# Optimization experiments

Measured on AMD Instinct MI355X. Metric: run time of the kernel, lower is better.

## Reference

```python
import jax, jax.numpy as jnp
import numpy as np

H = 256   # hidden_dim
S = 16    # d_state
B = 2
N = 8192
LN_EPS = 1e-5


def setup_inputs() -> dict:
    key = jax.random.key(0)
    ks = jax.random.split(key, 12)
    std = 1.0 / np.sqrt(H)
    inp = {
        'x': jax.random.normal(ks[0], (B, N, H), dtype=jnp.float32),
        'in_w': jax.random.normal(ks[1], (2 * H, H), dtype=jnp.float32) * std,
        'in_b': jax.random.normal(ks[2], (2 * H,), dtype=jnp.float32) * std,
        'xp_w': jax.random.normal(ks[3], (2 * S + 1, H), dtype=jnp.float32) * std,
        'xp_b': jax.random.normal(ks[4], (2 * S + 1,), dtype=jnp.float32) * std,
        'dt_w': jax.random.normal(ks[5], (H, 1), dtype=jnp.float32),
        'dt_b': jax.random.normal(ks[6], (H,), dtype=jnp.float32),
        'A_log': jnp.log(jnp.broadcast_to(jnp.arange(1, S + 1, dtype=jnp.float32), (H, S))),
        'D': jnp.ones((H,), dtype=jnp.float32),
        'out_w': jax.random.normal(ks[7], (H, H), dtype=jnp.float32) * std,
        'out_b': jax.random.normal(ks[8], (H,), dtype=jnp.float32) * std,
        'ln_g': jnp.ones((H,), dtype=jnp.float32),
        'ln_b': jnp.zeros((H,), dtype=jnp.float32),
    }
    return inp


def reference(x, in_w, in_b, xp_w, xp_b, dt_w, dt_b, A_log, D, out_w, out_b, ln_g, ln_b):
    # x: (B, N, H). Dropout is identity in eval mode.
    residual = x
    xz = jnp.einsum('bnh,kh->bnk', x, in_w) + in_b            # (B,N,2H)
    x_inner, z = xz[..., :H], xz[..., H:]
    x_dbl = jnp.einsum('bnh,kh->bnk', x_inner, xp_w) + xp_b   # (B,N,2S+1)
    dt_raw = x_dbl[..., :1]
    B_raw = x_dbl[..., 1:S + 1]                               # (B,N,S)
    C_raw = x_dbl[..., S + 1:]                                # (B,N,S)
    dt = jax.nn.softplus(dt_raw * dt_w[:, 0] + dt_b)          # (B,N,H)
    # NOTE: the original computes dA = exp(dt * A) but never uses it; A_log
    # does not affect the output, so we skip materializing dA.
    dB = dt[..., None] * B_raw[:, :, None, :]                 # (B,N,H,S)
    h = jnp.cumsum(x_inner[..., None] * dB, axis=1)           # (B,N,H,S)
    y = jnp.einsum('bnhs,bns->bnh', h, C_raw) + D * x_inner   # (B,N,H)
    y = y * jax.nn.silu(z)
    out = jnp.einsum('bnh,kh->bnk', y, out_w) + out_b
    r = out + residual
    mu = jnp.mean(r, axis=-1, keepdims=True)
    var = jnp.mean((r - mu) ** 2, axis=-1, keepdims=True)
    return ln_g * (r - mu) * jax.lax.rsqrt(var + LN_EPS) + ln_b
```

## Files before the change

kernel.cpp:

```cpp
#include <hip/hip_runtime.h>
#include <hip/hip_bf16.h>


#define HD 256
#define SD 16
#define NSEQ 8192
#define NBATCH 2
#define BN (NBATCH * NSEQ)
#define CHUNK 32
#define NCHUNK (NSEQ / CHUNK)
#define NGRP 16
#define GSZ (NCHUNK / NGRP)
#define LN_EPS 1e-5f

#define NIW (2 * HD * HD)
#define NXP (48 * HD)
#define NOW (HD * HD)

typedef __hip_bfloat16 bf16;
typedef __attribute__((ext_vector_type(8))) short bf16x8;
typedef __attribute__((ext_vector_type(4))) short short4v;
typedef __attribute__((ext_vector_type(4))) float f32x4;

__device__ __forceinline__ float b2f(bf16 v) { return __bfloat162float(v); }
__device__ __forceinline__ short f2bs(float f) {
  union { bf16 b; short s; } u;
  u.b = __float2bfloat16(f);
  return u.s;
}
__device__ __forceinline__ bf16x8 cvt_frag(const float* p) {
  bf16x8 r;
#pragma unroll
  for (int j = 0; j < 8; ++j) r[j] = f2bs(p[j]);
  return r;
}
__device__ __forceinline__ float softplus_f(float a) {
  return (a > 20.f) ? a : __logf(1.f + __expf(a));
}

__global__ __launch_bounds__(256) void k0_weights(
    const float* __restrict__ in_w, const float* __restrict__ xp_w,
    const float* __restrict__ out_w, bf16* __restrict__ wbin,
    bf16* __restrict__ wbxp, bf16* __restrict__ wbout)
{
  const int base = (blockIdx.x * 256 + threadIdx.x) * 4;
  if (base < NIW) {
    f32x4 v = *(const f32x4*)(in_w + base);
    *(short4v*)((short*)wbin + base) =
        short4v{f2bs(v[0]), f2bs(v[1]), f2bs(v[2]), f2bs(v[3])};
  } else if (base < NIW + NXP) {
    const int off = base - NIW;
    short4v s;
    if (off < 33 * HD) {
      f32x4 v = *(const f32x4*)(xp_w + off);
      s = short4v{f2bs(v[0]), f2bs(v[1]), f2bs(v[2]), f2bs(v[3])};
    } else {
      s = short4v{0, 0, 0, 0};
    }
    *(short4v*)((short*)wbxp + off) = s;
  } else if (base < NIW + NXP + NOW) {
    const int off = base - NIW - NXP;
    f32x4 v = *(const f32x4*)(out_w + off);
    *(short4v*)((short*)wbout + off) =
        short4v{f2bs(v[0]), f2bs(v[1]), f2bs(v[2]), f2bs(v[3])};
  }
}

__global__ __launch_bounds__(256) void k1f_in_xp_sum(
    const float* __restrict__ x, const bf16* __restrict__ wbin,
    const float* __restrict__ in_b, const bf16* __restrict__ wbxp,
    const float* __restrict__ xp_b, const float* __restrict__ dt_w,
    const float* __restrict__ dt_b, bf16* __restrict__ xib,
    bf16* __restrict__ zb, float* __restrict__ dbc, float* __restrict__ Mc)
{
  __shared__ float tile[32][260];
  __shared__ float sdbc[32][33];
  const int tid = threadIdx.x;
  const int wave = tid >> 6, lane = tid & 63, q = lane >> 4, l16 = lane & 15;
  const int R0 = blockIdx.x * CHUNK;

  f32x4 acc[2][8] = {};
  {
    const float* a0 = x + (size_t)(R0 + l16) * HD + q * 8;
    const float* a1 = a0 + 16 * HD;
    const bf16* bp = wbin + (size_t)(wave * 128 + l16) * HD + q * 8;
#pragma unroll
    for (int k = 0; k < HD; k += 32) {
      bf16x8 af0 = cvt_frag(a0 + k);
      bf16x8 af1 = cvt_frag(a1 + k);
#pragma unroll
      for (int t = 0; t < 8; ++t) {
        bf16x8 bfr = *(const bf16x8*)(bp + (size_t)t * 16 * HD + k);
        acc[0][t] = __builtin_amdgcn_mfma_f32_16x16x32_bf16(af0, bfr, acc[0][t], 0, 0, 0);
        acc[1][t] = __builtin_amdgcn_mfma_f32_16x16x32_bf16(af1, bfr, acc[1][t], 0, 0, 0);
      }
    }
  }
  if (wave < 2) {
#pragma unroll
    for (int t = 0; t < 8; ++t) {
      const int col = wave * 128 + t * 16 + l16;
      const float bias = in_b[col];
#pragma unroll
      for (int rt = 0; rt < 2; ++rt)
#pragma unroll
        for (int r = 0; r < 4; ++r)
          tile[rt * 16 + q * 4 + r][col] = acc[rt][t][r] + bias;
    }
  }
  __syncthreads();

  {
    const int row = tid >> 3;
    const int cb = (tid & 7) * 8;
#pragma unroll
    for (int j = 0; j < 4; ++j) {
      bf16x8 v = cvt_frag(&tile[row][cb + j * 64]);
      *(bf16x8*)(xib + (size_t)(R0 + row) * HD + cb + j * 64) = v;
    }
  }
  f32x4 pacc[3] = {};
  if (wave < 2) {
    const bf16* pb = wbxp + (size_t)l16 * HD + q * 8;
#pragma unroll
    for (int k = 0; k < HD; k += 32) {
      bf16x8 af = cvt_frag(&tile[wave * 16 + l16][k + q * 8]);
#pragma unroll
      for (int t = 0; t < 3; ++t) {
        bf16x8 bfr = *(const bf16x8*)(pb + (size_t)t * 16 * HD + k);
        pacc[t] = __builtin_amdgcn_mfma_f32_16x16x32_bf16(af, bfr, pacc[t], 0, 0, 0);
      }
    }
#pragma unroll
    for (int t = 0; t < 3; ++t) {
      const int col = t * 16 + l16;
      if (col < 33) {
        const float bias = xp_b[col];
#pragma unroll
        for (int r = 0; r < 4; ++r)
          sdbc[wave * 16 + q * 4 + r][col] = pacc[t][r] + bias;
      }
    }
  }
  __syncthreads();

  {
    const float* sflat = &sdbc[0][0];
    for (int idx = tid; idx < CHUNK * 33; idx += 256)
      dbc[(size_t)R0 * 33 + idx] = sflat[idx];
  }
  {
    const int h = tid;
    const float dtw = dt_w[h], dtb = dt_b[h];
    float st[SD] = {};
#pragma unroll
    for (int n = 0; n < CHUNK; ++n) {
      const float xv = tile[n][h];
      const float dt = softplus_f(sdbc[n][0] * dtw + dtb);
      const float u = xv * dt;
#pragma unroll
      for (int s = 0; s < SD; ++s) st[s] += u * sdbc[n][1 + s];
    }
    const int b = R0 >> 13, c = (R0 & (NSEQ - 1)) >> 5;
    float* mp = Mc + ((size_t)(b * NCHUNK + c)) * 4096 + h;
#pragma unroll
    for (int s = 0; s < SD; ++s) mp[s * HD] = st[s];
  }
  __syncthreads();

  if (wave >= 2) {
#pragma unroll
    for (int t = 0; t < 8; ++t) {
      const int gcol = wave * 128 + t * 16 + l16;
      const float bias = in_b[gcol];
      const int col = gcol - 256;
#pragma unroll
      for (int rt = 0; rt < 2; ++rt)
#pragma unroll
        for (int r = 0; r < 4; ++r)
          tile[rt * 16 + q * 4 + r][col] = acc[rt][t][r] + bias;
    }
  }
  __syncthreads();
  {
    const int row = tid >> 3;
    const int cb = (tid & 7) * 8;
#pragma unroll
    for (int j = 0; j < 4; ++j) {
      bf16x8 v = cvt_frag(&tile[row][cb + j * 64]);
      *(bf16x8*)(zb + (size_t)(R0 + row) * HD + cb + j * 64) = v;
    }
  }
}

__global__ __launch_bounds__(256) void k4a_prefix_local(
    float* __restrict__ Mc, float* __restrict__ Gs)
{
  const int tid = blockIdx.x * 256 + threadIdx.x;
  const int b = tid >> 16;
  const int g = (tid >> 12) & (NGRP - 1);
  const int hs = tid & 4095;
  float run = 0.f;
#pragma unroll
  for (int i = 0; i < GSZ; ++i) {
    const size_t idx = ((size_t)(b * NCHUNK + g * GSZ + i)) * 4096 + hs;
    const float v = Mc[idx];
    Mc[idx] = run;
    run += v;
  }
  Gs[((size_t)(b * NGRP + g)) * 4096 + hs] = run;
}

__global__ __launch_bounds__(256) void k4b_prefix_groups(float* __restrict__ Gs)
{
  const int tid = blockIdx.x * 256 + threadIdx.x;
  const int b = tid >> 12;
  const int hs = tid & 4095;
  float run = 0.f;
#pragma unroll
  for (int g = 0; g < NGRP; ++g) {
    const size_t idx = ((size_t)(b * NGRP + g)) * 4096 + hs;
    const float v = Gs[idx];
    Gs[idx] = run;
    run += v;
  }
}

__global__ __launch_bounds__(256) void k56_scan_out_ln(
    const bf16* __restrict__ xib, const bf16* __restrict__ zb,
    const float* __restrict__ dbc, const float* __restrict__ dt_w,
    const float* __restrict__ dt_b, const float* __restrict__ Dv,
    const float* __restrict__ Mc, const float* __restrict__ Gs,
    const bf16* __restrict__ wbout, const float* __restrict__ out_b,
    const float* __restrict__ x, const float* __restrict__ ln_g,
    const float* __restrict__ ln_b, float* __restrict__ out)
{
  __shared__ float sdbc[CHUNK][33];
  __shared__ float ytile[32][264];
  const int tid = threadIdx.x;
  const int R0 = blockIdx.x * CHUNK;
  const int b = R0 >> 13;
  const int cchunk = (R0 & (NSEQ - 1)) >> 5;

  for (int idx = tid; idx < CHUNK * 33; idx += 256) {
    const int n = idx / 33, j = idx - n * 33;
    sdbc[n][j] = dbc[(size_t)(R0 + n) * 33 + j];
  }
  __syncthreads();

  {
    const int h = tid;
    const float dtw = dt_w[h];
    const float dtb = dt_b[h];
    const float dv = Dv[h];
    float st[SD];
    const float* mp = Mc + ((size_t)(b * NCHUNK + cchunk)) * 4096 + h;
    const float* gp = Gs + ((size_t)(b * NGRP + cchunk / GSZ)) * 4096 + h;
#pragma unroll
    for (int s = 0; s < SD; ++s) st[s] = mp[s * HD] + gp[s * HD];
    for (int n = 0; n < CHUNK; ++n) {
      const size_t row = (size_t)(R0 + n) * HD + h;
      const float xv = b2f(xib[row]);
      const float zv = b2f(zb[row]);
      const float dt = softplus_f(sdbc[n][0] * dtw + dtb);
      const float u = xv * dt;
      float y = dv * xv;
#pragma unroll
      for (int s = 0; s < SD; ++s) {
        st[s] += u * sdbc[n][1 + s];
        y += st[s] * sdbc[n][17 + s];
      }
      const float sig = 1.f / (1.f + __expf(-zv));
      ytile[n][h] = y * zv * sig;
    }
  }
  __syncthreads();

  const int wave = tid >> 6;
  const int lane = tid & 63;
  const int q = lane >> 4;
  const int l16 = lane & 15;
  const int mrow = (wave & 1) * 16;
  const int colBase = (wave >> 1) * 128;

  f32x4 acc[8] = {};
  const bf16* bptr = wbout + (size_t)(colBase + l16) * HD + q * 8;
#pragma unroll
  for (int k = 0; k < HD; k += 32) {
    bf16x8 af = cvt_frag(&ytile[mrow + l16][k + q * 8]);
#pragma unroll
    for (int t = 0; t < 8; ++t) {
      bf16x8 bfr = *(const bf16x8*)(bptr + (size_t)t * 16 * HD + k);
      acc[t] = __builtin_amdgcn_mfma_f32_16x16x32_bf16(af, bfr, acc[t], 0, 0, 0);
    }
  }
  __syncthreads();

#pragma unroll
  for (int t = 0; t < 8; ++t) {
    const int col = colBase + t * 16 + l16;
    const float bias = out_b[col];
#pragma unroll
    for (int r = 0; r < 4; ++r) {
      const int row = mrow + q * 4 + r;
      ytile[row][col] = acc[t][r] + bias + x[(size_t)(R0 + row) * HD + col];
    }
  }
  __syncthreads();

#pragma unroll
  for (int rr = 0; rr < 8; ++rr) {
    const int row = wave * 8 + rr;
    float p = 0.f;
#pragma unroll
    for (int j = 0; j < 4; ++j) p += ytile[row][lane + 64 * j];
#pragma unroll
    for (int off = 32; off > 0; off >>= 1) p += __shfl_xor(p, off);
    const float mu = p * (1.f / 256.f);
    float v2 = 0.f;
#pragma unroll
    for (int j = 0; j < 4; ++j) {
      const float d = ytile[row][lane + 64 * j] - mu;
      v2 += d * d;
    }
#pragma unroll
    for (int off = 32; off > 0; off >>= 1) v2 += __shfl_xor(v2, off);
    const float rstd = rsqrtf(v2 * (1.f / 256.f) + LN_EPS);
    const size_t base = (size_t)(R0 + row) * HD;
#pragma unroll
    for (int j = 0; j < 4; ++j) {
      const int cc = lane + 64 * j;
      out[base + cc] = ln_g[cc] * (ytile[row][cc] - mu) * rstd + ln_b[cc];
    }
  }
}

extern "C" void kernel_launch(void* const* d_in, const int* in_sizes, int n_in,
                              void* d_out, int out_size, void* d_ws, size_t ws_size,
                              hipStream_t stream)
{
  const float* x     = (const float*)d_in[0];
  const float* in_w  = (const float*)d_in[1];
  const float* in_b  = (const float*)d_in[2];
  const float* xp_w  = (const float*)d_in[3];
  const float* xp_b  = (const float*)d_in[4];
  const float* dt_w  = (const float*)d_in[5];
  const float* dt_b  = (const float*)d_in[6];
  const float* Dv    = (const float*)d_in[8];
  const float* out_w = (const float*)d_in[9];
  const float* out_b = (const float*)d_in[10];
  const float* ln_g  = (const float*)d_in[11];
  const float* ln_b  = (const float*)d_in[12];

  char* ws = (char*)d_ws;
  bf16*  xib   = (bf16*)(ws);
  bf16*  zb    = (bf16*)(ws +  8388608);
  float* dbc   = (float*)(ws + 16777216);
  float* Mc    = (float*)(ws + 18939904);
  float* Gs    = (float*)(ws + 27328512);
  bf16*  wbin  = (bf16*)(ws + 27852800);
  bf16*  wbxp  = (bf16*)(ws + 28114944);
  bf16*  wbout = (bf16*)(ws + 28139520);
  float* out   = (float*)d_out;

  hipLaunchKernelGGL(k0_weights, dim3((NIW + NXP + NOW) / 1024), dim3(256),
                     0, stream, in_w, xp_w, out_w, wbin, wbxp, wbout);
  hipLaunchKernelGGL(k1f_in_xp_sum, dim3(BN / CHUNK), dim3(256), 0, stream,
                     x, wbin, in_b, wbxp, xp_b, dt_w, dt_b,
                     xib, zb, dbc, Mc);
  hipLaunchKernelGGL(k4a_prefix_local, dim3(NBATCH * NGRP * 4096 / 256),
                     dim3(256), 0, stream, Mc, Gs);
  hipLaunchKernelGGL(k4b_prefix_groups, dim3(NBATCH * 4096 / 256), dim3(256),
                     0, stream, Gs);
  hipLaunchKernelGGL(k56_scan_out_ln, dim3(BN / CHUNK), dim3(256), 0, stream,
                     xib, zb, dbc, dt_w, dt_b, Dv, Mc, Gs,
                     wbout, out_b, x, ln_g, ln_b, out);
}
```

Before: 167.5 us.

## Double block size to 512 threads, splitting state dimension across thread halves

Both the fused input-projection kernel and the scan/out-projection/LayerNorm kernel move from 256 to 512 threads per block. The 16 state channels are split between two thread halves, with partial y sums combined in shared memory. In the first kernel, x is staged in LDS and each wave computes a 16x128 tile, with x and z written through separate tiles. The goal is more parallelism and fewer serial state updates per thread, at the cost of more LDS per block, extra syncs and a reduction pass.

```diff
diff --git a/kernel.cpp b/kernel.cpp
--- a/kernel.cpp
+++ b/kernel.cpp
@@ -66,65 +66,78 @@
   }
 }
 
-__global__ __launch_bounds__(256) void k1f_in_xp_sum(
+__global__ __launch_bounds__(512) void k1f_in_xp_sum(
     const float* __restrict__ x, const bf16* __restrict__ wbin,
     const float* __restrict__ in_b, const bf16* __restrict__ wbxp,
     const float* __restrict__ xp_b, const float* __restrict__ dt_w,
     const float* __restrict__ dt_b, bf16* __restrict__ xib,
     bf16* __restrict__ zb, float* __restrict__ dbc, float* __restrict__ Mc)
 {
-  __shared__ float tile[32][260];
+  __shared__ float xt[32][260];
+  __shared__ float zt[32][260];
   __shared__ float sdbc[32][33];
   const int tid = threadIdx.x;
   const int wave = tid >> 6, lane = tid & 63, q = lane >> 4, l16 = lane & 15;
   const int R0 = blockIdx.x * CHUNK;
 
-  f32x4 acc[2][8] = {};
-  {
-    const float* a0 = x + (size_t)(R0 + l16) * HD + q * 8;
-    const float* a1 = a0 + 16 * HD;
-    const bf16* bp = wbin + (size_t)(wave * 128 + l16) * HD + q * 8;
+  {
+    const int row = tid >> 4;
+    const int c0 = (tid & 15) * 16;
+    const float* src = x + (size_t)(R0 + row) * HD + c0;
+#pragma unroll
+    for (int j = 0; j < 4; ++j)
+      *(f32x4*)&xt[row][c0 + j * 4] = *(const f32x4*)(src + j * 4);
+  }
+  __syncthreads();
+
+  const int mrow = (wave & 1) * 16;
+  const int colBase = (wave >> 1) * 128;
+  f32x4 acc[8] = {};
+  {
+    const bf16* bp = wbin + (size_t)(colBase + l16) * HD + q * 8;
 #pragma unroll
     for (int k = 0; k < HD; k += 32) {
-      bf16x8 af0 = cvt_frag(a0 + k);
-      bf16x8 af1 = cvt_frag(a1 + k);
+      bf16x8 af = cvt_frag(&xt[mrow + l16][k + q * 8]);
 #pragma unroll
       for (int t = 0; t < 8; ++t) {
         bf16x8 bfr = *(const bf16x8*)(bp + (size_t)t * 16 * HD + k);
-        acc[0][t] = __builtin_amdgcn_mfma_f32_16x16x32_bf16(af0, bfr, acc[0][t], 0, 0, 0);
-        acc[1][t] = __builtin_amdgcn_mfma_f32_16x16x32_bf16(af1, bfr, acc[1][t], 0, 0, 0);
-      }
-    }
-  }
+        acc[t] = __builtin_amdgcn_mfma_f32_16x16x32_bf16(af, bfr, acc[t], 0, 0, 0);
+      }
+    }
+  }
+  __syncthreads();
+
+  {
+    float (*dst)[260] = (wave < 4) ? xt : zt;
+    const int cb = (wave < 4) ? colBase : (colBase - 256);
+#pragma unroll
+    for (int t = 0; t < 8; ++t) {
+      const int gcol = colBase + t * 16 + l16;
+      const float bias = in_b[gcol];
+#pragma unroll
+      for (int r = 0; r < 4; ++r)
+        dst[mrow + q * 4 + r][cb + t * 16 + l16] = acc[t][r] + bias;
+    }
+  }
+  __syncthreads();
+
+  {
+    const int row = tid >> 4;
+    const int c0 = (tid & 15) * 16;
+    bf16* xd = xib + (size_t)(R0 + row) * HD + c0;
+    bf16* zd = zb + (size_t)(R0 + row) * HD + c0;
+    *(bf16x8*)xd = cvt_frag(&xt[row][c0]);
+    *(bf16x8*)(xd + 8) = cvt_frag(&xt[row][c0 + 8]);
+    *(bf16x8*)zd = cvt_frag(&zt[row][c0]);
+    *(bf16x8*)(zd + 8) = cvt_frag(&zt[row][c0 + 8]);
+  }
+
   if (wave < 2) {
-#pragma unroll
-    for (int t = 0; t < 8; ++t) {
-      const int col = wave * 128 + t * 16 + l16;
-      const float bias = in_b[col];
-#pragma unroll
-      for (int rt = 0; rt < 2; ++rt)
-#pragma unroll
-        for (int r = 0; r < 4; ++r)
-          tile[rt * 16 + q * 4 + r][col] = acc[rt][t][r] + bias;
-    }
-  }
-  __syncthreads();
-
-  {
-    const int row = tid >> 3;
-    const int cb = (tid & 7) * 8;
-#pragma unroll
-    for (int j = 0; j < 4; ++j) {
-      bf16x8 v = cvt_frag(&tile[row][cb + j * 64]);
-      *(bf16x8*)(xib + (size_t)(R0 + row) * HD + cb + j * 64) = v;
-    }
-  }
-  f32x4 pacc[3] = {};
-  if (wave < 2) {
+    f32x4 pacc[3] = {};
     const bf16* pb = wbxp + (size_t)l16 * HD + q * 8;
 #pragma unroll
     for (int k = 0; k < HD; k += 32) {
-      bf16x8 af = cvt_frag(&tile[wave * 16 + l16][k + q * 8]);
+      bf16x8 af = cvt_frag(&xt[wave * 16 + l16][k + q * 8]);
 #pragma unroll
       for (int t = 0; t < 3; ++t) {
         bf16x8 bfr = *(const bf16x8*)(pb + (size_t)t * 16 * HD + k);
@@ -146,50 +159,26 @@
 
   {
     const float* sflat = &sdbc[0][0];
-    for (int idx = tid; idx < CHUNK * 33; idx += 256)
+    for (int idx = tid; idx < CHUNK * 33; idx += 512)
       dbc[(size_t)R0 * 33 + idx] = sflat[idx];
   }
   {
-    const int h = tid;
+    const int h = tid & 255;
+    const int sh = tid >> 8;
     const float dtw = dt_w[h], dtb = dt_b[h];
-    float st[SD] = {};
+    float st[8] = {};
 #pragma unroll
     for (int n = 0; n < CHUNK; ++n) {
-      const float xv = tile[n][h];
+      const float xv = xt[n][h];
       const float dt = softplus_f(sdbc[n][0] * dtw + dtb);
       const float u = xv * dt;
 #pragma unroll
-      for (int s = 0; s < SD; ++s) st[s] += u * sdbc[n][1 + s];
+      for (int s = 0; s < 8; ++s) st[s] += u * sdbc[n][1 + sh * 8 + s];
     }
     const int b = R0 >> 13, c = (R0 & (NSEQ - 1)) >> 5;
-    float* mp = Mc + ((size_t)(b * NCHUNK + c)) * 4096 + h;
-#pragma unroll
-    for (int s = 0; s < SD; ++s) mp[s * HD] = st[s];
-  }
-  __syncthreads();
-
-  if (wave >= 2) {
-#pragma unroll
-    for (int t = 0; t < 8; ++t) {
-      const int gcol = wave * 128 + t * 16 + l16;
-      const float bias = in_b[gcol];
-      const int col = gcol - 256;
-#pragma unroll
-      for (int rt = 0; rt < 2; ++rt)
-#pragma unroll
-        for (int r = 0; r < 4; ++r)
-          tile[rt * 16 + q * 4 + r][col] = acc[rt][t][r] + bias;
-    }
-  }
-  __syncthreads();
-  {
-    const int row = tid >> 3;
-    const int cb = (tid & 7) * 8;
-#pragma unroll
-    for (int j = 0; j < 4; ++j) {
-      bf16x8 v = cvt_frag(&tile[row][cb + j * 64]);
-      *(bf16x8*)(zb + (size_t)(R0 + row) * HD + cb + j * 64) = v;
-    }
+    float* mp = Mc + ((size_t)(b * NCHUNK + c)) * 4096 + (sh * 8) * HD + h;
+#pragma unroll
+    for (int s = 0; s < 8; ++s) mp[s * HD] = st[s];
   }
 }
 
@@ -226,7 +215,7 @@
   }
 }
 
-__global__ __launch_bounds__(256) void k56_scan_out_ln(
+__global__ __launch_bounds__(512) void k56_scan_out_ln(
     const bf16* __restrict__ xib, const bf16* __restrict__ zb,
     const float* __restrict__ dbc, const float* __restrict__ dt_w,
     const float* __restrict__ dt_b, const float* __restrict__ Dv,
@@ -236,91 +225,101 @@
     const float* __restrict__ ln_b, float* __restrict__ out)
 {
   __shared__ float sdbc[CHUNK][33];
-  __shared__ float ytile[32][264];
+  __shared__ float yt[32][260];
+  __shared__ float pt[32][260];
   const int tid = threadIdx.x;
+  const int wave = tid >> 6, lane = tid & 63, q = lane >> 4, l16 = lane & 15;
   const int R0 = blockIdx.x * CHUNK;
   const int b = R0 >> 13;
   const int cchunk = (R0 & (NSEQ - 1)) >> 5;
 
-  for (int idx = tid; idx < CHUNK * 33; idx += 256) {
+  for (int idx = tid; idx < CHUNK * 33; idx += 512) {
     const int n = idx / 33, j = idx - n * 33;
     sdbc[n][j] = dbc[(size_t)(R0 + n) * 33 + j];
   }
   __syncthreads();
 
   {
-    const int h = tid;
-    const float dtw = dt_w[h];
-    const float dtb = dt_b[h];
+    const int h = tid & 255;
+    const int sh = tid >> 8;
+    const float dtw = dt_w[h], dtb = dt_b[h];
     const float dv = Dv[h];
-    float st[SD];
-    const float* mp = Mc + ((size_t)(b * NCHUNK + cchunk)) * 4096 + h;
-    const float* gp = Gs + ((size_t)(b * NGRP + cchunk / GSZ)) * 4096 + h;
-#pragma unroll
-    for (int s = 0; s < SD; ++s) st[s] = mp[s * HD] + gp[s * HD];
+    float st[8];
+    const float* mp = Mc + ((size_t)(b * NCHUNK + cchunk)) * 4096 + sh * 8 * HD + h;
+    const float* gp = Gs + ((size_t)(b * NGRP + cchunk / GSZ)) * 4096 + sh * 8 * HD + h;
+#pragma unroll
+    for (int s = 0; s < 8; ++s) st[s] = mp[s * HD] + gp[s * HD];
+    float (*dst)[260] = (sh == 0) ? yt : pt;
     for (int n = 0; n < CHUNK; ++n) {
-      const size_t row = (size_t)(R0 + n) * HD + h;
-      const float xv = b2f(xib[row]);
-      const float zv = b2f(zb[row]);
+      const float xv = b2f(xib[(size_t)(R0 + n) * HD + h]);
       const float dt = softplus_f(sdbc[n][0] * dtw + dtb);
       const float u = xv * dt;
-      float y = dv * xv;
-#pragma unroll
-      for (int s = 0; s < SD; ++s) {
-        st[s] += u * sdbc[n][1 + s];
-        y += st[s] * sdbc[n][17 + s];
-      }
+      float y = (sh == 0) ? dv * xv : 0.f;
+#pragma unroll
+      for (int s = 0; s < 8; ++s) {
+        st[s] += u * sdbc[n][1 + sh * 8 + s];
+        y += st[s] * sdbc[n][17 + sh * 8 + s];
+      }
+      dst[n][h] = y;
+    }
+  }
+  __syncthreads();
+
+  {
+    const int h = tid & 255;
+    const int r2 = tid >> 8;
+#pragma unroll
+    for (int j = 0; j < 16; ++j) {
+      const int row = r2 * 16 + j;
+      const float zv = b2f(zb[(size_t)(R0 + row) * HD + h]);
       const float sig = 1.f / (1.f + __expf(-zv));
-      ytile[n][h] = y * zv * sig;
-    }
-  }
-  __syncthreads();
-
-  const int wave = tid >> 6;
-  const int lane = tid & 63;
-  const int q = lane >> 4;
-  const int l16 = lane & 15;
+      yt[row][h] = (yt[row][h] + pt[row][h]) * zv * sig;
+    }
+  }
+  __syncthreads();
+
   const int mrow = (wave & 1) * 16;
-  const int colBase = (wave >> 1) * 128;
-
-  f32x4 acc[8] = {};
-  const bf16* bptr = wbout + (size_t)(colBase + l16) * HD + q * 8;
-#pragma unroll
-  for (int k = 0; k < HD; k += 32) {
-    bf16x8 af = cvt_frag(&ytile[mrow + l16][k + q * 8]);
-#pragma unroll
-    for (int t = 0; t < 8; ++t) {
-      bf16x8 bfr = *(const bf16x8*)(bptr + (size_t)t * 16 * HD + k);
-      acc[t] = __builtin_amdgcn_mfma_f32_16x16x32_bf16(af, bfr, acc[t], 0, 0, 0);
-    }
-  }
-  __syncthreads();
-
-#pragma unroll
-  for (int t = 0; t < 8; ++t) {
+  const int colBase = (wave >> 1) * 64;
+  f32x4 acc[4] = {};
+  {
+    const bf16* bp = wbout + (size_t)(colBase + l16) * HD + q * 8;
+#pragma unroll
+    for (int k = 0; k < HD; k += 32) {
+      bf16x8 af = cvt_frag(&yt[mrow + l16][k + q * 8]);
+#pragma unroll
+      for (int t = 0; t < 4; ++t) {
+        bf16x8 bfr = *(const bf16x8*)(bp + (size_t)t * 16 * HD + k);
+        acc[t] = __builtin_amdgcn_mfma_f32_16x16x32_bf16(af, bfr, acc[t], 0, 0, 0);
+      }
+    }
+  }
+  __syncthreads();
+
+#pragma unroll
+  for (int t = 0; t < 4; ++t) {
     const int col = colBase + t * 16 + l16;
     const float bias = out_b[col];
 #pragma unroll
     for (int r = 0; r < 4; ++r) {
       const int row = mrow + q * 4 + r;
-      ytile[row][col] = acc[t][r] + bias + x[(size_t)(R0 + row) * HD + col];
-    }
-  }
-  __syncthreads();
-
-#pragma unroll
-  for (int rr = 0; rr < 8; ++rr) {
-    const int row = wave * 8 + rr;
+      pt[row][col] = acc[t][r] + bias + x[(size_t)(R0 + row) * HD + col];
+    }
+  }
+  __syncthreads();
+
+#pragma unroll
+  for (int rr = 0; rr < 4; ++rr) {
+    const int row = wave * 4 + rr;
     float p = 0.f;
 #pragma unroll
-    for (int j = 0; j < 4; ++j) p += ytile[row][lane + 64 * j];
+    for (int j = 0; j < 4; ++j) p += pt[row][lane + 64 * j];
 #pragma unroll
     for (int off = 32; off > 0; off >>= 1) p += __shfl_xor(p, off);
     const float mu = p * (1.f / 256.f);
     float v2 = 0.f;
 #pragma unroll
     for (int j = 0; j < 4; ++j) {
-      const float d = ytile[row][lane + 64 * j] - mu;
+      const float d = pt[row][lane + 64 * j] - mu;
       v2 += d * d;
     }
 #pragma unroll
@@ -330,7 +329,7 @@
 #pragma unroll
     for (int j = 0; j < 4; ++j) {
       const int cc = lane + 64 * j;
-      out[base + cc] = ln_g[cc] * (ytile[row][cc] - mu) * rstd + ln_b[cc];
+      out[base + cc] = ln_g[cc] * (pt[row][cc] - mu) * rstd + ln_b[cc];
     }
   }
 }
@@ -365,14 +364,14 @@
 
   hipLaunchKernelGGL(k0_weights, dim3((NIW + NXP + NOW) / 1024), dim3(256),
                      0, stream, in_w, xp_w, out_w, wbin, wbxp, wbout);
-  hipLaunchKernelGGL(k1f_in_xp_sum, dim3(BN / CHUNK), dim3(256), 0, stream,
+  hipLaunchKernelGGL(k1f_in_xp_sum, dim3(BN / CHUNK), dim3(512), 0, stream,
                      x, wbin, in_b, wbxp, xp_b, dt_w, dt_b,
                      xib, zb, dbc, Mc);
   hipLaunchKernelGGL(k4a_prefix_local, dim3(NBATCH * NGRP * 4096 / 256),
                      dim3(256), 0, stream, Mc, Gs);
   hipLaunchKernelGGL(k4b_prefix_groups, dim3(NBATCH * 4096 / 256), dim3(256),
                      0, stream, Gs);
-  hipLaunchKernelGGL(k56_scan_out_ln, dim3(BN / CHUNK), dim3(256), 0, stream,
+  hipLaunchKernelGGL(k56_scan_out_ln, dim3(BN / CHUNK), dim3(512), 0, stream,
                      xib, zb, dbc, dt_w, dt_b, Dv, Mc, Gs,
                      wbout, out_b, x, ln_g, ln_b, out);
 }
```

After: 169.5 us. About the same (+1.2%).
